# Kernel optimization log

Hardware: AMD Instinct MI355X
Metric: run time of the kernel (lower is better)

## Reference

```python
import jax, jax.numpy as jnp
import numpy as np

H = 1024  # hidden_size
I = 1024  # input_size
C = 64    # hidden_channel == out_channel
B = 1     # batch_size


def act(x):
    # CustomActivation: (|x+1| - |x-1|) / 2  == clamp(x, -1, 1)
    return (jnp.abs(x + 1.0) - jnp.abs(x - 1.0)) * 0.5


def setup_inputs() -> dict:
    key = jax.random.key(0)
    ks = jax.random.split(key, 8)
    x = jax.random.normal(ks[0], (B * C, H, I), dtype=jnp.float32)
    p_mask = jax.random.normal(ks[1], (H, I), dtype=jnp.float32)
    Wp = jnp.tril(jax.random.normal(ks[2], (H, H), dtype=jnp.float32))
    Wp = Wp.at[jnp.arange(H), jnp.arange(H)].set(1.0)
    Wp_diag = jnp.ones((H,), dtype=jnp.float32)
    Wzp = jax.random.normal(ks[3], (H, H), dtype=jnp.float32)
    lim = 1.0 / np.sqrt(I)
    p_lin_w = jax.random.uniform(ks[4], (I, I), minval=-lim, maxval=lim, dtype=jnp.float32)
    p_lin_b = jnp.zeros((I,), dtype=jnp.float32)
    z_lin_w = jax.random.uniform(ks[5], (I, I), minval=-lim, maxval=lim, dtype=jnp.float32)
    z_lin_b = jnp.zeros((I,), dtype=jnp.float32)
    return {"x": x, "p_mask": p_mask, "Wp": Wp, "Wp_diag": Wp_diag, "Wzp": Wzp,
            "p_lin_w": p_lin_w, "p_lin_b": p_lin_b, "z_lin_w": z_lin_w, "z_lin_b": z_lin_b}


def reference(x, p_mask, Wp, Wp_diag, Wzp, p_lin_w, p_lin_b, z_lin_w, z_lin_b):
    # x: (C, H, I) since batch_size == 1
    # in-place no_grad processing of Wp: tril + clamp diagonal to [0,1]
    Wp_proc = jnp.tril(Wp)
    diag = jnp.clip(jnp.diagonal(Wp_proc), 0.0, 1.0)
    Wp_proc = Wp_proc.at[jnp.arange(H), jnp.arange(H)].set(diag)
    # torch mutates .data under no_grad, so grad w.r.t. Wp is identity through this step
    Wp_eff = Wp + jax.lax.stop_gradient(Wp_proc - Wp) + jnp.diag(Wp_diag)

    p_set = x * act(p_mask)  # (C, H, I), mask broadcast over channels

    # per-channel Wp @ p_set[i], batched over channels
    t = jnp.einsum('hk,cki->chi', Wp_eff, p_set)
    # p_output_layer: act -> Linear(I, I) -> act   (Linear acts on last dim)
    p_out = act(jnp.einsum('chi,ji->chj', act(t), p_lin_w) + p_lin_b)

    z = jnp.einsum('hk,cki->chi', Wzp, p_out)
    z_out = act(jnp.einsum('chi,ji->chj', act(z), z_lin_w) + z_lin_b)

    out = (p_out + z_out).reshape(B, C, H, I)  # out_channel == hidden_channel
    return out
```

## Files before the change

kernel.cpp:

```cpp
#include <hip/hip_runtime.h>
#include <hip/hip_bf16.h>


typedef short bf16x8 __attribute__((ext_vector_type(8)));
typedef float f32x4  __attribute__((ext_vector_type(4)));

__device__ __forceinline__ float actf(float v) { return fminf(1.f, fmaxf(-1.f, v)); }

__device__ __forceinline__ unsigned short f2bf(float f) {
    union { __hip_bfloat16 b; unsigned short u; } cv;
    cv.b = __float2bfloat16(f);
    return cv.u;
}
__device__ __forceinline__ float bf2f(unsigned short u) {
    union { unsigned short u; __hip_bfloat16 b; } cv;
    cv.u = u;
    return __bfloat162float(cv.b);
}

__device__ __forceinline__ int swz(int r) { return (r ^ (r >> 2)) & 3; }

__device__ __forceinline__ void stage_tile(const unsigned short* __restrict__ g,
                                           int row0, int k0,
                                           unsigned short* ldsBase, int t) {
    const int wave = t >> 6;
#pragma unroll
    for (int s = 0; s < 2; ++s) {
        const int ci = s * 256 + t;
        const int r  = ci >> 2;
        const int pc = ci & 3;
        const int q  = pc ^ swz(r);
        const unsigned short* gsrc = g + ((size_t)(row0 + r) << 10) + k0 + q * 8;
        unsigned short* ldst = ldsBase + (size_t)(s * 256 + wave * 64) * 8;
        __builtin_amdgcn_global_load_lds((const __attribute__((address_space(1))) void*)gsrc,
                                         (__attribute__((address_space(3))) void*)ldst,
                                         16, 0, 0);
    }
}

__device__ __forceinline__ bf16x8 read_frag(const unsigned short* ldsBase, int row, int q) {
    const int pc = q ^ swz(row);
    return *(const bf16x8*)(ldsBase + row * 32 + pc * 8);
}

template <bool SPLIT, int EPI, bool TRIL>
__global__ __launch_bounds__(256)
void gemm_tn(const unsigned short* __restrict__ Ahi,
             const unsigned short* __restrict__ Alo,
             const unsigned short* __restrict__ Bhi,
             const unsigned short* __restrict__ Blo,
             const float* __restrict__ bias,
             const unsigned short* __restrict__ Phi,
             const unsigned short* __restrict__ Plo,
             unsigned short* __restrict__ O1,
             unsigned short* __restrict__ O2,
             float* __restrict__ Of) {
    __shared__ __align__(16) unsigned short lds[(SPLIT ? 4 : 2) * 4096];
    unsigned short* ldsAhi = lds;
    unsigned short* ldsBhi = lds + 4096;
    unsigned short* ldsAlo = lds + (SPLIT ? 8192 : 0);
    unsigned short* ldsBlo = lds + (SPLIT ? 12288 : 0);

    const int t    = threadIdx.x;
    const int lane = t & 63;
    const int wave = t >> 6;
    const int wm = wave >> 1, wn = wave & 1;
    const int q = lane >> 4, mr = lane & 15;

    const int m0 = blockIdx.y * 128;
    const int n0 = blockIdx.x * 128;
    const size_t cb = (size_t)blockIdx.z << 20;

    const unsigned short* Bh = Bhi + cb;
    const unsigned short* Bl = Blo + cb;

    f32x4 acc[4][4];
#pragma unroll
    for (int i = 0; i < 4; ++i)
#pragma unroll
        for (int j = 0; j < 4; ++j) acc[i][j] = (f32x4){0.f, 0.f, 0.f, 0.f};

    const int kEnd = TRIL ? ((m0 + 128 < 1024) ? m0 + 128 : 1024) : 1024;

    for (int k0 = 0; k0 < kEnd; k0 += 32) {
        __syncthreads();
        stage_tile(Ahi, m0, k0, ldsAhi, t);
        stage_tile(Bh,  n0, k0, ldsBhi, t);
        if constexpr (SPLIT) {
            stage_tile(Alo, m0, k0, ldsAlo, t);
            stage_tile(Bl,  n0, k0, ldsBlo, t);
        }
        __syncthreads();

        bf16x8 aH[4], bH[4], aL[4], bL[4];
#pragma unroll
        for (int i = 0; i < 4; ++i) {
            aH[i] = read_frag(ldsAhi, wm * 64 + i * 16 + mr, q);
            bH[i] = read_frag(ldsBhi, wn * 64 + i * 16 + mr, q);
            if constexpr (SPLIT) {
                aL[i] = read_frag(ldsAlo, wm * 64 + i * 16 + mr, q);
                bL[i] = read_frag(ldsBlo, wn * 64 + i * 16 + mr, q);
            }
        }
#pragma unroll
        for (int i = 0; i < 4; ++i)
#pragma unroll
            for (int j = 0; j < 4; ++j) {
                if constexpr (SPLIT) {
                    acc[i][j] = __builtin_amdgcn_mfma_f32_16x16x32_bf16(aL[i], bH[j], acc[i][j], 0, 0, 0);
                    acc[i][j] = __builtin_amdgcn_mfma_f32_16x16x32_bf16(aH[i], bL[j], acc[i][j], 0, 0, 0);
                }
                acc[i][j] = __builtin_amdgcn_mfma_f32_16x16x32_bf16(aH[i], bH[j], acc[i][j], 0, 0, 0);
            }
    }

#pragma unroll
    for (int i = 0; i < 4; ++i) {
        const int gmBase = m0 + wm * 64 + i * 16 + q * 4;
#pragma unroll
        for (int j = 0; j < 4; ++j) {
            const int gn = n0 + wn * 64 + j * 16 + mr;
#pragma unroll
            for (int r4 = 0; r4 < 4; ++r4) {
                const int gm = gmBase + r4;
                const size_t off = cb + ((size_t)gm << 10) + gn;
                float v = acc[i][j][r4];
                if constexpr (EPI == 0) {
                    O1[off] = f2bf(actf(v));
                } else if constexpr (EPI == 1) {
                    v = actf(v + bias[gm]);
                    const unsigned short hi = f2bf(v);
                    O1[off] = hi;
                    O2[off] = f2bf(v - bf2f(hi));
                } else {
                    v = actf(v + bias[gm]);
                    v += bf2f(Phi[off]) + bf2f(Plo[off]);
                    Of[off] = v;
                }
            }
        }
    }
}

__global__ void prep_weights(const float* __restrict__ Wp, const float* __restrict__ Wpd,
                             const float* __restrict__ Wzp,
                             const float* __restrict__ plw, const float* __restrict__ zlw,
                             unsigned short* __restrict__ WpHi, unsigned short* __restrict__ WpLo,
                             unsigned short* __restrict__ WzHi, unsigned short* __restrict__ WzLo,
                             unsigned short* __restrict__ plw16, unsigned short* __restrict__ zlw16) {
    const int idx = blockIdx.x * 256 + threadIdx.x;
    const int h = idx >> 10, k = idx & 1023;
    float v = (k < h) ? Wp[idx] : 0.f;
    if (k == h) v = fminf(1.f, fmaxf(0.f, Wp[idx])) + Wpd[h];
    unsigned short hi = f2bf(v);
    WpHi[idx] = hi; WpLo[idx] = f2bf(v - bf2f(hi));
    const float wz = Wzp[idx];
    hi = f2bf(wz);
    WzHi[idx] = hi; WzLo[idx] = f2bf(wz - bf2f(hi));
    plw16[idx] = f2bf(plw[idx]);
    zlw16[idx] = f2bf(zlw[idx]);
}

__global__ void prep_pset(const float* __restrict__ x, const float* __restrict__ pmask,
                          unsigned short* __restrict__ Thi, unsigned short* __restrict__ Tlo) {
    __shared__ float tile[32][33];
    const int tx = threadIdx.x, ty = threadIdx.y;
    const int i0 = blockIdx.x * 32, h0 = blockIdx.y * 32;
    const size_t cb = (size_t)blockIdx.z << 20;
#pragma unroll
    for (int s = 0; s < 4; ++s) {
        const int hh = ty + s * 8;
        const size_t gi = ((size_t)(h0 + hh) << 10) + i0 + tx;
        tile[hh][tx] = x[cb + gi] * actf(pmask[gi]);
    }
    __syncthreads();
#pragma unroll
    for (int s = 0; s < 4; ++s) {
        const int ii = ty + s * 8;
        const float v = tile[tx][ii];
        const size_t go = cb + ((size_t)(i0 + ii) << 10) + h0 + tx;
        const unsigned short hi = f2bf(v);
        Thi[go] = hi;
        Tlo[go] = f2bf(v - bf2f(hi));
    }
}

__global__ void transpose_out(const float* __restrict__ inT,
                              float* __restrict__ out) {
    __shared__ float tile[32][33];
    const int tx = threadIdx.x, ty = threadIdx.y;
    const int h0 = blockIdx.x * 32, j0 = blockIdx.y * 32;
    const size_t cb = (size_t)blockIdx.z << 20;
#pragma unroll
    for (int s = 0; s < 4; ++s) {
        const int jj = ty + s * 8;
        tile[jj][tx] = inT[cb + ((size_t)(j0 + jj) << 10) + h0 + tx];
    }
    __syncthreads();
#pragma unroll
    for (int s = 0; s < 4; ++s) {
        const int hh = ty + s * 8;
        out[cb + ((size_t)(h0 + hh) << 10) + j0 + tx] = tile[tx][hh];
    }
}

extern "C" void kernel_launch(void* const* d_in, const int* in_sizes, int n_in,
                              void* d_out, int out_size, void* d_ws, size_t ws_size,
                              hipStream_t stream) {
    const float* x     = (const float*)d_in[0];
    const float* pmask = (const float*)d_in[1];
    const float* Wp    = (const float*)d_in[2];
    const float* Wpd   = (const float*)d_in[3];
    const float* Wzp   = (const float*)d_in[4];
    const float* plw   = (const float*)d_in[5];
    const float* plb   = (const float*)d_in[6];
    const float* zlw   = (const float*)d_in[7];
    const float* zlb   = (const float*)d_in[8];
    float* out = (float*)d_out;

    char* w = (char*)d_ws;
    const size_t SZ = 134217728ull;
    unsigned short* pSetT_hi = (unsigned short*)(w);
    unsigned short* pSetT_lo = (unsigned short*)(w + SZ);
    unsigned short* pT_hi    = (unsigned short*)(w + 2 * SZ);
    unsigned short* pT_lo    = (unsigned short*)(w + 3 * SZ);
    unsigned short* tA       = (unsigned short*)(w + 4 * SZ);
    float*          outT     = (float*)(w);
    unsigned short* wts      = (unsigned short*)(w + 5 * SZ);
    unsigned short* WpHi = wts;
    unsigned short* WpLo = wts + 1 * 1048576;
    unsigned short* WzHi = wts + 2 * 1048576;
    unsigned short* WzLo = wts + 3 * 1048576;
    unsigned short* plw16 = wts + 4 * 1048576;
    unsigned short* zlw16 = wts + 5 * 1048576;

    const dim3 gW(4096), bW(256);
    const dim3 gT(32, 32, 64), bT(32, 8);
    const dim3 gG(8, 8, 64), bG(256);

    prep_weights<<<gW, bW, 0, stream>>>(Wp, Wpd, Wzp, plw, zlw,
                                        WpHi, WpLo, WzHi, WzLo, plw16, zlw16);
    prep_pset<<<gT, bT, 0, stream>>>(x, pmask, pSetT_hi, pSetT_lo);

    gemm_tn<true, 0, true><<<gG, bG, 0, stream>>>(
        WpHi, WpLo, pSetT_hi, pSetT_lo, nullptr, nullptr, nullptr, tA, nullptr, nullptr);

    gemm_tn<false, 1, false><<<gG, bG, 0, stream>>>(
        plw16, nullptr, tA, nullptr, plb, nullptr, nullptr, pT_hi, pT_lo, nullptr);

    gemm_tn<true, 0, false><<<gG, bG, 0, stream>>>(
        WzHi, WzLo, pT_hi, pT_lo, nullptr, nullptr, nullptr, tA, nullptr, nullptr);

    gemm_tn<false, 2, false><<<gG, bG, 0, stream>>>(
        zlw16, nullptr, tA, nullptr, zlb, pT_hi, pT_lo, nullptr, nullptr, outT);

    transpose_out<<<gT, bT, 0, stream>>>(outT, out);
}
```

Before: 1.853 ms.

## Use 256x256 tiles with 8 waves and double-buffered LDS prefetch in GEMMs

Replaces the 128x128, 4-wave GEMM with a 256x256, 8-wave kernel. It double-buffers the LDS tiles and spreads the next tile's global-to-LDS loads across four MFMA sub-phases, using vmcnt waits, barriers and setprio. This is meant to hide global load latency behind MFMA work and halve operand reloads per flop. In exchange it uses more LDS (up to 128 KB for the split case), more accumulator registers, and far fewer blocks, so occupancy and the TRIL load balance may suffer.

```diff
diff --git a/kernel.cpp b/kernel.cpp
--- a/kernel.cpp
+++ b/kernel.cpp
@@ -20,103 +20,219 @@
 
 __device__ __forceinline__ int swz(int r) { return (r ^ (r >> 2)) & 3; }
 
-__device__ __forceinline__ void stage_tile(const unsigned short* __restrict__ g,
-                                           int row0, int k0,
-                                           unsigned short* ldsBase, int t) {
-    const int wave = t >> 6;
-#pragma unroll
-    for (int s = 0; s < 2; ++s) {
-        const int ci = s * 256 + t;
+__device__ __forceinline__ bf16x8 read_frag(const unsigned short* ldsBase, int row, int q) {
+    const int pc = q ^ swz(row);
+    return *(const bf16x8*)(ldsBase + row * 32 + pc * 8);
+}
+
+template <bool SPLIT, int EPI, bool TRIL>
+__global__ __launch_bounds__(512, 2)
+void gemm_tn8(const unsigned short* __restrict__ Ahi,
+              const unsigned short* __restrict__ Alo,
+              const unsigned short* __restrict__ Bhi,
+              const unsigned short* __restrict__ Blo,
+              const float* __restrict__ bias,
+              const unsigned short* __restrict__ Phi,
+              const unsigned short* __restrict__ Plo,
+              unsigned short* __restrict__ O1,
+              unsigned short* __restrict__ O2,
+              float* __restrict__ Of) {
+    constexpr int NOPS   = SPLIT ? 4 : 2;
+    constexpr int ROUNDS = SPLIT ? 8 : 4;
+    __shared__ __align__(16) unsigned short lds[NOPS * 2 * 8192];
+
+    const int tid  = threadIdx.x;
+    const int lane = tid & 63;
+    const int wave = tid >> 6;
+    const int wm = wave >> 2;
+    const int wn = wave & 3;
+    const int q  = lane >> 4;
+    const int mr = lane & 15;
+
+    const int m0 = blockIdx.y * 256;
+    const int n0 = blockIdx.x * 256;
+    const size_t cb = (size_t)blockIdx.z << 20;
+
+    const unsigned short* Bh = Bhi + cb;
+    const unsigned short* Bl = SPLIT ? (Blo + cb) : nullptr;
+
+    auto stage1 = [&](const unsigned short* g, int row0, int k0,
+                      unsigned short* base, int rnd) {
+        const int ci = rnd * 512 + tid;
         const int r  = ci >> 2;
         const int pc = ci & 3;
-        const int q  = pc ^ swz(r);
-        const unsigned short* gsrc = g + ((size_t)(row0 + r) << 10) + k0 + q * 8;
-        unsigned short* ldst = ldsBase + (size_t)(s * 256 + wave * 64) * 8;
+        const int qq = pc ^ swz(r);
+        const unsigned short* gsrc = g + ((size_t)(row0 + r) << 10) + k0 + qq * 8;
+        unsigned short* ldst = base + (rnd * 512 + wave * 64) * 8;
         __builtin_amdgcn_global_load_lds((const __attribute__((address_space(1))) void*)gsrc,
                                          (__attribute__((address_space(3))) void*)ldst,
                                          16, 0, 0);
-    }
-}
-
-__device__ __forceinline__ bf16x8 read_frag(const unsigned short* ldsBase, int row, int q) {
-    const int pc = q ^ swz(row);
-    return *(const bf16x8*)(ldsBase + row * 32 + pc * 8);
-}
-
-template <bool SPLIT, int EPI, bool TRIL>
-__global__ __launch_bounds__(256)
-void gemm_tn(const unsigned short* __restrict__ Ahi,
-             const unsigned short* __restrict__ Alo,
-             const unsigned short* __restrict__ Bhi,
-             const unsigned short* __restrict__ Blo,
-             const float* __restrict__ bias,
-             const unsigned short* __restrict__ Phi,
-             const unsigned short* __restrict__ Plo,
-             unsigned short* __restrict__ O1,
-             unsigned short* __restrict__ O2,
-             float* __restrict__ Of) {
-    __shared__ __align__(16) unsigned short lds[(SPLIT ? 4 : 2) * 4096];
-    unsigned short* ldsAhi = lds;
-    unsigned short* ldsBhi = lds + 4096;
-    unsigned short* ldsAlo = lds + (SPLIT ? 8192 : 0);
-    unsigned short* ldsBlo = lds + (SPLIT ? 12288 : 0);
-
-    const int t    = threadIdx.x;
-    const int lane = t & 63;
-    const int wave = t >> 6;
-    const int wm = wave >> 1, wn = wave & 1;
-    const int q = lane >> 4, mr = lane & 15;
-
-    const int m0 = blockIdx.y * 128;
-    const int n0 = blockIdx.x * 128;
-    const size_t cb = (size_t)blockIdx.z << 20;
-
-    const unsigned short* Bh = Bhi + cb;
-    const unsigned short* Bl = Blo + cb;
-
-    f32x4 acc[4][4];
-#pragma unroll
-    for (int i = 0; i < 4; ++i)
+    };
+    auto issueRound = [&](int idx, int k0, int buf) {
+        int op, rnd;
+        if constexpr (SPLIT) { op = (idx & 1) + ((idx >= 4) ? 2 : 0); rnd = (idx >> 1) & 1; }
+        else                 { op = idx & 1; rnd = idx >> 1; }
+        const unsigned short* g; int row0;
+        switch (op) {
+            case 0:  g = Ahi; row0 = m0; break;
+            case 1:  g = Bh;  row0 = n0; break;
+            case 2:  g = Alo; row0 = m0; break;
+            default: g = Bl;  row0 = n0; break;
+        }
+        stage1(g, row0, k0, lds + (op * 2 + buf) * 8192, rnd);
+    };
+
+    f32x4 acc[8][4];
+#pragma unroll
+    for (int i = 0; i < 8; ++i)
 #pragma unroll
         for (int j = 0; j < 4; ++j) acc[i][j] = (f32x4){0.f, 0.f, 0.f, 0.f};
 
-    const int kEnd = TRIL ? ((m0 + 128 < 1024) ? m0 + 128 : 1024) : 1024;
-
-    for (int k0 = 0; k0 < kEnd; k0 += 32) {
-        __syncthreads();
-        stage_tile(Ahi, m0, k0, ldsAhi, t);
-        stage_tile(Bh,  n0, k0, ldsBhi, t);
-        if constexpr (SPLIT) {
-            stage_tile(Alo, m0, k0, ldsAlo, t);
-            stage_tile(Bl,  n0, k0, ldsBlo, t);
-        }
-        __syncthreads();
-
-        bf16x8 aH[4], bH[4], aL[4], bL[4];
-#pragma unroll
-        for (int i = 0; i < 4; ++i) {
-            aH[i] = read_frag(ldsAhi, wm * 64 + i * 16 + mr, q);
-            bH[i] = read_frag(ldsBhi, wn * 64 + i * 16 + mr, q);
+    const int kEnd = TRIL ? ((m0 + 256 < 1024) ? m0 + 256 : 1024) : 1024;
+    const int nt = kEnd >> 5;
+
+#pragma unroll
+    for (int idx = 0; idx < ROUNDS; ++idx) issueRound(idx, 0, 0);
+
+    for (int t = 0; t < nt; ++t) {
+        const int cur = t & 1;
+        const int nxt = cur ^ 1;
+        const int k0n = (t + 1) << 5;
+        const bool pf = (t + 1) < nt;
+
+        const unsigned short* Ah_ = lds + (0 * 2 + cur) * 8192;
+        const unsigned short* Bh_ = lds + (1 * 2 + cur) * 8192;
+        const unsigned short* Al_ = SPLIT ? (lds + (2 * 2 + cur) * 8192) : nullptr;
+        const unsigned short* Bl_ = SPLIT ? (lds + (3 * 2 + cur) * 8192) : nullptr;
+
+        if (pf) {
+            issueRound(0, k0n, nxt);
+            issueRound(1, k0n, nxt);
+            asm volatile("s_waitcnt vmcnt(2)" ::: "memory");
+        } else {
+            asm volatile("s_waitcnt vmcnt(0)" ::: "memory");
+        }
+        asm volatile("s_barrier" ::: "memory");
+
+        bf16x8 bh01[2], bl01[2], bh23[2], bl23[2];
+
+        {
+            bf16x8 aH[4], aL[4];
+#pragma unroll
+            for (int i = 0; i < 4; ++i) {
+                aH[i] = read_frag(Ah_, wm * 128 + i * 16 + mr, q);
+                if constexpr (SPLIT) aL[i] = read_frag(Al_, wm * 128 + i * 16 + mr, q);
+            }
+#pragma unroll
+            for (int j = 0; j < 2; ++j) {
+                bh01[j] = read_frag(Bh_, wn * 64 + j * 16 + mr, q);
+                if constexpr (SPLIT) bl01[j] = read_frag(Bl_, wn * 64 + j * 16 + mr, q);
+            }
+            if (pf) { issueRound(2, k0n, nxt); issueRound(3, k0n, nxt); }
+            asm volatile("s_barrier" ::: "memory");
+            __builtin_amdgcn_s_setprio(1);
+#pragma unroll
+            for (int i = 0; i < 4; ++i)
+#pragma unroll
+                for (int j = 0; j < 2; ++j) {
+                    if constexpr (SPLIT) {
+                        acc[i][j] = __builtin_amdgcn_mfma_f32_16x16x32_bf16(aL[i], bh01[j], acc[i][j], 0, 0, 0);
+                        acc[i][j] = __builtin_amdgcn_mfma_f32_16x16x32_bf16(aH[i], bl01[j], acc[i][j], 0, 0, 0);
+                    }
+                    acc[i][j] = __builtin_amdgcn_mfma_f32_16x16x32_bf16(aH[i], bh01[j], acc[i][j], 0, 0, 0);
+                }
+            __builtin_amdgcn_s_setprio(0);
+            __builtin_amdgcn_sched_barrier(0);
+            asm volatile("s_barrier" ::: "memory");
+        }
+
+        {
+            bf16x8 aH[4], aL[4];
+#pragma unroll
+            for (int i = 0; i < 4; ++i) {
+                aH[i] = read_frag(Ah_, wm * 128 + 64 + i * 16 + mr, q);
+                if constexpr (SPLIT) aL[i] = read_frag(Al_, wm * 128 + 64 + i * 16 + mr, q);
+            }
             if constexpr (SPLIT) {
-                aL[i] = read_frag(ldsAlo, wm * 64 + i * 16 + mr, q);
-                bL[i] = read_frag(ldsBlo, wn * 64 + i * 16 + mr, q);
-            }
-        }
-#pragma unroll
-        for (int i = 0; i < 4; ++i)
-#pragma unroll
-            for (int j = 0; j < 4; ++j) {
-                if constexpr (SPLIT) {
-                    acc[i][j] = __builtin_amdgcn_mfma_f32_16x16x32_bf16(aL[i], bH[j], acc[i][j], 0, 0, 0);
-                    acc[i][j] = __builtin_amdgcn_mfma_f32_16x16x32_bf16(aH[i], bL[j], acc[i][j], 0, 0, 0);
-                }
-                acc[i][j] = __builtin_amdgcn_mfma_f32_16x16x32_bf16(aH[i], bH[j], acc[i][j], 0, 0, 0);
-            }
-    }
-
-#pragma unroll
-    for (int i = 0; i < 4; ++i) {
-        const int gmBase = m0 + wm * 64 + i * 16 + q * 4;
+                if (pf) { issueRound(4, k0n, nxt); issueRound(5, k0n, nxt); }
+            }
+            asm volatile("s_barrier" ::: "memory");
+            __builtin_amdgcn_s_setprio(1);
+#pragma unroll
+            for (int i = 0; i < 4; ++i)
+#pragma unroll
+                for (int j = 0; j < 2; ++j) {
+                    if constexpr (SPLIT) {
+                        acc[i + 4][j] = __builtin_amdgcn_mfma_f32_16x16x32_bf16(aL[i], bh01[j], acc[i + 4][j], 0, 0, 0);
+                        acc[i + 4][j] = __builtin_amdgcn_mfma_f32_16x16x32_bf16(aH[i], bl01[j], acc[i + 4][j], 0, 0, 0);
+                    }
+                    acc[i + 4][j] = __builtin_amdgcn_mfma_f32_16x16x32_bf16(aH[i], bh01[j], acc[i + 4][j], 0, 0, 0);
+                }
+            __builtin_amdgcn_s_setprio(0);
+            __builtin_amdgcn_sched_barrier(0);
+            asm volatile("s_barrier" ::: "memory");
+        }
+
+        {
+            bf16x8 aH[4], aL[4];
+#pragma unroll
+            for (int i = 0; i < 4; ++i) {
+                aH[i] = read_frag(Ah_, wm * 128 + i * 16 + mr, q);
+                if constexpr (SPLIT) aL[i] = read_frag(Al_, wm * 128 + i * 16 + mr, q);
+            }
+#pragma unroll
+            for (int j = 0; j < 2; ++j) {
+                bh23[j] = read_frag(Bh_, wn * 64 + (j + 2) * 16 + mr, q);
+                if constexpr (SPLIT) bl23[j] = read_frag(Bl_, wn * 64 + (j + 2) * 16 + mr, q);
+            }
+            if constexpr (SPLIT) {
+                if (pf) { issueRound(6, k0n, nxt); issueRound(7, k0n, nxt); }
+            }
+            asm volatile("s_barrier" ::: "memory");
+            __builtin_amdgcn_s_setprio(1);
+#pragma unroll
+            for (int i = 0; i < 4; ++i)
+#pragma unroll
+                for (int j = 0; j < 2; ++j) {
+                    if constexpr (SPLIT) {
+                        acc[i][j + 2] = __builtin_amdgcn_mfma_f32_16x16x32_bf16(aL[i], bh23[j], acc[i][j + 2], 0, 0, 0);
+                        acc[i][j + 2] = __builtin_amdgcn_mfma_f32_16x16x32_bf16(aH[i], bl23[j], acc[i][j + 2], 0, 0, 0);
+                    }
+                    acc[i][j + 2] = __builtin_amdgcn_mfma_f32_16x16x32_bf16(aH[i], bh23[j], acc[i][j + 2], 0, 0, 0);
+                }
+            __builtin_amdgcn_s_setprio(0);
+            __builtin_amdgcn_sched_barrier(0);
+            asm volatile("s_barrier" ::: "memory");
+        }
+
+        {
+            bf16x8 aH[4], aL[4];
+#pragma unroll
+            for (int i = 0; i < 4; ++i) {
+                aH[i] = read_frag(Ah_, wm * 128 + 64 + i * 16 + mr, q);
+                if constexpr (SPLIT) aL[i] = read_frag(Al_, wm * 128 + 64 + i * 16 + mr, q);
+            }
+            asm volatile("s_barrier" ::: "memory");
+            __builtin_amdgcn_s_setprio(1);
+#pragma unroll
+            for (int i = 0; i < 4; ++i)
+#pragma unroll
+                for (int j = 0; j < 2; ++j) {
+                    if constexpr (SPLIT) {
+                        acc[i + 4][j + 2] = __builtin_amdgcn_mfma_f32_16x16x32_bf16(aL[i], bh23[j], acc[i + 4][j + 2], 0, 0, 0);
+                        acc[i + 4][j + 2] = __builtin_amdgcn_mfma_f32_16x16x32_bf16(aH[i], bl23[j], acc[i + 4][j + 2], 0, 0, 0);
+                    }
+                    acc[i + 4][j + 2] = __builtin_amdgcn_mfma_f32_16x16x32_bf16(aH[i], bh23[j], acc[i + 4][j + 2], 0, 0, 0);
+                }
+            __builtin_amdgcn_s_setprio(0);
+            __builtin_amdgcn_sched_barrier(0);
+            asm volatile("s_barrier" ::: "memory");
+        }
+    }
+
+#pragma unroll
+    for (int i = 0; i < 8; ++i) {
+        const int gmBase = m0 + wm * 128 + i * 16 + q * 4;
 #pragma unroll
         for (int j = 0; j < 4; ++j) {
             const int gn = n0 + wn * 64 + j * 16 + mr;
@@ -236,22 +352,22 @@
 
     const dim3 gW(4096), bW(256);
     const dim3 gT(32, 32, 64), bT(32, 8);
-    const dim3 gG(8, 8, 64), bG(256);
+    const dim3 gG(4, 4, 64), bG(512);
 
     prep_weights<<<gW, bW, 0, stream>>>(Wp, Wpd, Wzp, plw, zlw,
                                         WpHi, WpLo, WzHi, WzLo, plw16, zlw16);
     prep_pset<<<gT, bT, 0, stream>>>(x, pmask, pSetT_hi, pSetT_lo);
 
-    gemm_tn<true, 0, true><<<gG, bG, 0, stream>>>(
+    gemm_tn8<true, 0, true><<<gG, bG, 0, stream>>>(
         WpHi, WpLo, pSetT_hi, pSetT_lo, nullptr, nullptr, nullptr, tA, nullptr, nullptr);
 
-    gemm_tn<false, 1, false><<<gG, bG, 0, stream>>>(
+    gemm_tn8<false, 1, false><<<gG, bG, 0, stream>>>(
         plw16, nullptr, tA, nullptr, plb, nullptr, nullptr, pT_hi, pT_lo, nullptr);
 
-    gemm_tn<true, 0, false><<<gG, bG, 0, stream>>>(
+    gemm_tn8<true, 0, false><<<gG, bG, 0, stream>>>(
         WzHi, WzLo, pT_hi, pT_lo, nullptr, nullptr, nullptr, tA, nullptr, nullptr);
 
-    gemm_tn<false, 2, false><<<gG, bG, 0, stream>>>(
+    gemm_tn8<false, 2, false><<<gG, bG, 0, stream>>>(
         zlw16, nullptr, tA, nullptr, zlb, pT_hi, pT_lo, nullptr, nullptr, outT);
 
     transpose_out<<<gT, bT, 0, stream>>>(outT, out);
```

New measurement: 1.783 ms. 1.04x faster.
